# Optimization experiments

Measured on AMD Instinct MI355X. Metric: run time of the kernel, lower is better.

The kernel has to match this reference:

```python
import jax, jax.numpy as jnp
import numpy as np

BATCH, N_NODES = 256, 128
NF = MF = 128
EF = AEF = 5


def setup_inputs() -> dict:
    key = jax.random.key(0)
    k = jax.random.split(key, 6)
    afm = jax.random.normal(k[0], (BATCH, N_NODES, NF), dtype=jnp.float32)
    bfm = jax.random.randint(k[1], (BATCH, N_NODES, N_NODES), 0, EF + 1, dtype=jnp.int32)
    a_bfm = jax.random.randint(k[2], (BATCH, N_NODES), 0, AEF + 1, dtype=jnp.int32)
    adj = jax.random.uniform(k[3], (BATCH, N_NODES, N_NODES), dtype=jnp.float32)
    # xavier_uniform for adj_w (ef, mf, nf): fan_in=nf, fan_out=mf per torch convention on last two dims
    lim_w = float(np.sqrt(6.0 / (MF + NF)))
    adj_w = jax.random.uniform(k[4], (EF, MF, NF), minval=-lim_w, maxval=lim_w, dtype=jnp.float32)
    lim_a = float(np.sqrt(6.0 / (AEF + MF)))
    adj_a = jax.random.uniform(k[5], (AEF, MF), minval=-lim_a, maxval=lim_a, dtype=jnp.float32)
    return {"afm": afm, "bfm": bfm, "a_bfm": a_bfm, "adj": adj, "adj_w": adj_w, "adj_a": adj_a}


def reference(afm, bfm, a_bfm, adj, adj_w, adj_a):
    # afm is accepted by the original forward but never used.
    E = adj_w.shape[0] + 1  # zeros row for "no edge" at index 0
    mf, nf = adj_w.shape[1], adj_w.shape[2]
    W_ext = jnp.concatenate([jnp.zeros((1, mf, nf), adj_w.dtype), adj_w], axis=0)  # (E, mf, nf)
    A_ext = jnp.concatenate([jnp.zeros((1, mf), adj_a.dtype), adj_a], axis=0)      # (E_a, mf)
    att = A_ext[a_bfm]  # (b, n, mf); nf == mf required by original matmul
    # Original: msg[b,i,j,m] = sum_k W_ext[bfm[b,i,j], m, k] * att[b, j, k], then sum over i.
    # Contract first per edge type (small), then count-weight instead of gathering huge tensor.
    contrib = jnp.einsum('emn,bjn->bjem', W_ext, att)                  # (b, n, E, mf)
    cnt = jax.nn.one_hot(bfm, E, dtype=contrib.dtype).sum(axis=1)      # (b, j, E) = #{i : bfm[b,i,j]=e}
    messages = jnp.einsum('bje,bjem->bjm', cnt, contrib)               # (b, n, mf)
    return jnp.matmul(adj, messages)                                   # (b, n, mf)
```

## Files before the change

### kernel.cpp

```cpp
#include <hip/hip_runtime.h>

typedef short s16x8 __attribute__((ext_vector_type(8)));
typedef float f32x4 __attribute__((ext_vector_type(4)));
typedef int i32x4 __attribute__((ext_vector_type(4)));

__device__ __forceinline__ short f2bf(float f) {
  union { float f; unsigned u; } cv;
  cv.f = f;
  unsigned u = cv.u;
  u = (u + 0x7FFFu + ((u >> 16) & 1u)) >> 16;
  return (short)u;
}
__device__ __forceinline__ unsigned pk2(float lo, float hi) {
  union { float f; unsigned u; } a, b;
  a.f = lo;
  b.f = hi;
  return (a.u >> 16) | (b.u & 0xFFFF0000u);
}

__global__ __launch_bounds__(256, 4) void hist_mc_kernel(
    const int* __restrict__ bfm, const float* __restrict__ adj_w,
    const float* __restrict__ adj_a, uint2* __restrict__ cnt_h,
    unsigned short* __restrict__ McT) {
  __shared__ unsigned red[4][32][4][2];
  __shared__ float As[5][128];
  const int t = threadIdx.x;

  if (blockIdx.x < 20) {
    const int bi = blockIdx.x;
    const int e = bi >> 2, mg = bi & 3;
    for (int idx = t; idx < 640; idx += 256) As[idx >> 7][idx & 127] = adj_a[idx];
    __syncthreads();
    const int m = mg * 32 + (t >> 3), ns = t & 7;
    const float* W = adj_w + (size_t)e * 16384 + (size_t)m * 128 + ns * 16;
    float acc[5] = {0.f, 0.f, 0.f, 0.f, 0.f};
#pragma unroll
    for (int it = 0; it < 4; ++it) {
      const float4 wv = *(const float4*)(W + it * 4);
      const float wa[4] = {wv.x, wv.y, wv.z, wv.w};
#pragma unroll
      for (int q = 0; q < 4; ++q) {
        const int n = ns * 16 + it * 4 + q;
#pragma unroll
        for (int a = 0; a < 5; ++a) acc[a] = fmaf(wa[q], As[a][n], acc[a]);
      }
    }
#pragma unroll
    for (int d = 1; d < 8; d <<= 1)
#pragma unroll
      for (int a = 0; a < 5; ++a) acc[a] += __shfl_xor(acc[a], d);
    if (ns == 0) {
#pragma unroll
      for (int a = 0; a < 5; ++a)
        McT[m * 40 + e * 5 + a] = (unsigned short)f2bf(acc[a]);
      if (e == 0)
#pragma unroll
        for (int r = 25; r < 40; ++r) McT[m * 40 + r] = 0;
    }
    return;
  }

  const int idx2 = blockIdx.x - 20;
  const int b = idx2 >> 1, hh = idx2 & 1;
  const int w = t >> 6, l = t & 63;
  const i32x4* bp = (const i32x4*)bfm + (size_t)b * 4096 + hh * 2048;
  unsigned pA[4] = {0, 0, 0, 0}, pB[4] = {0, 0, 0, 0};
#pragma unroll
  for (int it = 0; it < 8; ++it) {
    const i32x4 v = __builtin_nontemporal_load(&bp[it * 256 + t]);
#pragma unroll
    for (int jj = 0; jj < 4; ++jj) {
      const int vj = v[jj];
      pA[jj] += (unsigned)(vj == 1) + ((unsigned)(vj == 2) << 8) +
                ((unsigned)(vj == 3) << 16) + ((unsigned)(vj == 4) << 24);
      pB[jj] += (unsigned)(vj == 5);
    }
  }
#pragma unroll
  for (int jj = 0; jj < 4; ++jj) {
    pA[jj] += (unsigned)__shfl_xor((int)pA[jj], 32);
    pB[jj] += (unsigned)__shfl_xor((int)pB[jj], 32);
  }
  if (l < 32) {
#pragma unroll
    for (int jj = 0; jj < 4; ++jj) {
      red[w][l][jj][0] = pA[jj];
      red[w][l][jj][1] = pB[jj];
    }
  }
  __syncthreads();
  if (t < 128) {
    unsigned A = 0, B = 0;
    const int cc = t >> 2, jj = t & 3;
#pragma unroll
    for (int w2 = 0; w2 < 4; ++w2) {
      A += red[w2][cc][jj][0];
      B += red[w2][cc][jj][1];
    }
    cnt_h[(b * 2 + hh) * 128 + t] = make_uint2(A, B);
  }
}

__global__ __launch_bounds__(256, 2) void skinny_kernel(
    const float* __restrict__ adj, const int* __restrict__ a_bfm,
    const uint2* __restrict__ cnt_h, const unsigned short* __restrict__ McT,
    float* __restrict__ out) {
  __shared__ __align__(16) unsigned short Pt[32 * 128];
  __shared__ __align__(16) unsigned short Mt[128 * 40];
  __shared__ __align__(16) unsigned short Qs[4 * 16 * 40];
  const int bh = blockIdx.x, b = bh >> 1, hh = bh & 1;
  const int t = threadIdx.x, w = t >> 6, l = t & 63, g = l >> 4, c = l & 15;
  const int row0 = hh * 64 + w * 16;

  uint2 h0 = make_uint2(0u, 0u), h1 = make_uint2(0u, 0u);
  int av = 0;
  if (t < 128) {
    h0 = cnt_h[(b * 2 + 0) * 128 + t];
    h1 = cnt_h[(b * 2 + 1) * 128 + t];
    av = a_bfm[b * 128 + t];
  }
  s16x8 mst0 = *(const s16x8*)&McT[t * 8];
  s16x8 mst1 = *(const s16x8*)&McT[(256 + t) * 8];
  s16x8 mst2 = {0, 0, 0, 0, 0, 0, 0, 0};
  if (t < 128) mst2 = *(const s16x8*)&McT[(512 + t) * 8];
  const float* arow = adj + (size_t)b * 16384 + (size_t)(row0 + c) * 128;
  f32x4 a0[4], a1[4];
#pragma unroll
  for (int kk = 0; kk < 4; ++kk) {
    a0[kk] = __builtin_nontemporal_load(
        (const f32x4*)(arow + kk * 32 + g * 8));
    a1[kk] = __builtin_nontemporal_load(
        (const f32x4*)(arow + kk * 32 + g * 8 + 4));
  }

  ((uint4*)Pt)[t] = make_uint4(0u, 0u, 0u, 0u);
  ((uint4*)Pt)[256 + t] = make_uint4(0u, 0u, 0u, 0u);
  *(s16x8*)&Mt[t * 8] = mst0;
  *(s16x8*)&Mt[(256 + t) * 8] = mst1;
  if (t < 128) *(s16x8*)&Mt[(512 + t) * 8] = mst2;
  asm volatile("s_waitcnt lgkmcnt(0)" ::: "memory");
  __builtin_amdgcn_s_barrier();

  if (t < 128 && av > 0) {
    const unsigned cx = h0.x + h1.x;
    const unsigned cy = h0.y + h1.y;
    const int ai = av - 1;
    const int chunk = t >> 3, off = t & 7;
    const float cf[5] = {(float)(cx & 255u), (float)((cx >> 8) & 255u),
                         (float)((cx >> 16) & 255u), (float)(cx >> 24),
                         (float)(cy & 255u)};
#pragma unroll
    for (int ei = 0; ei < 5; ++ei) {
      const int r = ei * 5 + ai;
      Pt[r * 128 + ((chunk ^ (r & 15)) << 3) + off] =
          (unsigned short)f2bf(cf[ei]);
    }
  }
  asm volatile("s_waitcnt lgkmcnt(0)" ::: "memory");
  __builtin_amdgcn_s_barrier();

  s16x8 bP[4][2];
#pragma unroll
  for (int kk = 0; kk < 4; ++kk)
#pragma unroll
    for (int ct = 0; ct < 2; ++ct) {
      const int r = ct * 16 + c;
      bP[kk][ct] = *(const s16x8*)&Pt[r * 128 + (((kk * 4 + g) ^ (r & 15)) << 3)];
    }
  s16x8 apk[4];
#pragma unroll
  for (int kk = 0; kk < 4; ++kk) {
    unsigned* pu = (unsigned*)&apk[kk];
    pu[0] = pk2(a0[kk][0], a0[kk][1]);
    pu[1] = pk2(a0[kk][2], a0[kk][3]);
    pu[2] = pk2(a1[kk][0], a1[kk][1]);
    pu[3] = pk2(a1[kk][2], a1[kk][3]);
  }
  f32x4 accQ[2] = {{0.f, 0.f, 0.f, 0.f}, {0.f, 0.f, 0.f, 0.f}};
#pragma unroll
  for (int kk = 0; kk < 4; ++kk)
#pragma unroll
    for (int ct = 0; ct < 2; ++ct)
      accQ[ct] = __builtin_amdgcn_mfma_f32_16x16x32_bf16(apk[kk], bP[kk][ct],
                                                         accQ[ct], 0, 0, 0);

  unsigned short* qsw = &Qs[w * 16 * 40];
#pragma unroll
  for (int ct = 0; ct < 2; ++ct)
#pragma unroll
    for (int q = 0; q < 4; ++q)
      qsw[(g * 4 + q) * 40 + ct * 16 + c] = (unsigned short)f2bf(accQ[ct][q]);
  const s16x8 aQ = *(const s16x8*)&qsw[c * 40 + g * 8];

  float* ob = out + (size_t)b * 16384 + (size_t)row0 * 128;
#pragma unroll
  for (int mt = 0; mt < 8; ++mt) {
    const s16x8 bM = *(const s16x8*)&Mt[(mt * 16 + c) * 40 + g * 8];
    f32x4 acc2 = {0.f, 0.f, 0.f, 0.f};
    acc2 = __builtin_amdgcn_mfma_f32_16x16x32_bf16(aQ, bM, acc2, 0, 0, 0);
#pragma unroll
    for (int q = 0; q < 4; ++q)
      __builtin_nontemporal_store(acc2[q],
                                  &ob[(g * 4 + q) * 128 + mt * 16 + c]);
  }
}

extern "C" void kernel_launch(void* const* d_in, const int* in_sizes, int n_in,
                              void* d_out, int out_size, void* d_ws,
                              size_t ws_size, hipStream_t stream) {
  const int* bfm = (const int*)d_in[1];
  const int* a_bfm = (const int*)d_in[2];
  const float* adj = (const float*)d_in[3];
  const float* adj_w = (const float*)d_in[4];
  const float* adj_a = (const float*)d_in[5];
  float* out = (float*)d_out;

  unsigned short* McT = (unsigned short*)d_ws;
  uint2* cnt_h = (uint2*)((char*)d_ws + 16384);

  hist_mc_kernel<<<dim3(532), dim3(256), 0, stream>>>(bfm, adj_w, adj_a,
                                                      cnt_h, McT);
  skinny_kernel<<<dim3(512), dim3(256), 0, stream>>>(adj, a_bfm, cnt_h, McT,
                                                     out);
}
```

Before: 16.86 us.

## Spread adj_w·adj_a precompute across all histogram blocks instead of dedicated blocks

The 20 dedicated blocks that computed the per-edge-type weight/attention products are removed. Each of the 640 (m,e) dot products is now handled by one wave in waves 0-1 of the 512 histogram blocks, using a 64-lane shuffle reduction. The bfm loads are also issued up front into registers so they overlap with this extra work. This evens out the tail of the first kernel and cuts the grid to 512 blocks, at the cost of more registers and more shuffle work per block.

```diff
diff --git a/kernel.cpp b/kernel.cpp
--- a/kernel.cpp
+++ b/kernel.cpp
@@ -23,54 +23,61 @@
     const float* __restrict__ adj_a, uint2* __restrict__ cnt_h,
     unsigned short* __restrict__ McT) {
   __shared__ unsigned red[4][32][4][2];
-  __shared__ float As[5][128];
   const int t = threadIdx.x;
-
-  if (blockIdx.x < 20) {
-    const int bi = blockIdx.x;
-    const int e = bi >> 2, mg = bi & 3;
-    for (int idx = t; idx < 640; idx += 256) As[idx >> 7][idx & 127] = adj_a[idx];
-    __syncthreads();
-    const int m = mg * 32 + (t >> 3), ns = t & 7;
-    const float* W = adj_w + (size_t)e * 16384 + (size_t)m * 128 + ns * 16;
-    float acc[5] = {0.f, 0.f, 0.f, 0.f, 0.f};
-#pragma unroll
-    for (int it = 0; it < 4; ++it) {
-      const float4 wv = *(const float4*)(W + it * 4);
-      const float wa[4] = {wv.x, wv.y, wv.z, wv.w};
-#pragma unroll
-      for (int q = 0; q < 4; ++q) {
-        const int n = ns * 16 + it * 4 + q;
-#pragma unroll
-        for (int a = 0; a < 5; ++a) acc[a] = fmaf(wa[q], As[a][n], acc[a]);
-      }
-    }
-#pragma unroll
-    for (int d = 1; d < 8; d <<= 1)
+  const int bid = blockIdx.x;
+  const int b = bid >> 1, hh = bid & 1;
+  const int w = t >> 6, l = t & 63;
+
+  int p = -1;
+  float2 wv = make_float2(0.f, 0.f);
+  float2 av2[5];
+#pragma unroll
+  for (int a = 0; a < 5; ++a) av2[a] = make_float2(0.f, 0.f);
+  if (w < 2) {
+    const int pc = bid + (w << 9);
+    if (pc < 640) {
+      p = pc;
+      const int e = pc % 5, m = pc / 5;
+      wv = *(const float2*)(adj_w + (size_t)e * 16384 + (size_t)m * 128 + l * 2);
+#pragma unroll
+      for (int a = 0; a < 5; ++a)
+        av2[a] = *(const float2*)(adj_a + a * 128 + l * 2);
+    }
+  }
+
+  const i32x4* bp = (const i32x4*)bfm + (size_t)b * 4096 + hh * 2048;
+  i32x4 bv[8];
+#pragma unroll
+  for (int it = 0; it < 8; ++it)
+    bv[it] = __builtin_nontemporal_load(&bp[it * 256 + t]);
+
+  if (p >= 0) {
+    float acc[5];
+#pragma unroll
+    for (int a = 0; a < 5; ++a) acc[a] = wv.x * av2[a].x + wv.y * av2[a].y;
+#pragma unroll
+    for (int d = 1; d < 64; d <<= 1)
 #pragma unroll
       for (int a = 0; a < 5; ++a) acc[a] += __shfl_xor(acc[a], d);
-    if (ns == 0) {
+    if (l == 0) {
+      const int e = p % 5, m = p / 5;
 #pragma unroll
       for (int a = 0; a < 5; ++a)
         McT[m * 40 + e * 5 + a] = (unsigned short)f2bf(acc[a]);
-      if (e == 0)
-#pragma unroll
-        for (int r = 25; r < 40; ++r) McT[m * 40 + r] = 0;
-    }
-    return;
-  }
-
-  const int idx2 = blockIdx.x - 20;
-  const int b = idx2 >> 1, hh = idx2 & 1;
-  const int w = t >> 6, l = t & 63;
-  const i32x4* bp = (const i32x4*)bfm + (size_t)b * 4096 + hh * 2048;
+    }
+  }
+  if (bid == 511 && t >= 128) {
+    const int m = t - 128;
+#pragma unroll
+    for (int r = 25; r < 40; ++r) McT[m * 40 + r] = 0;
+  }
+
   unsigned pA[4] = {0, 0, 0, 0}, pB[4] = {0, 0, 0, 0};
 #pragma unroll
   for (int it = 0; it < 8; ++it) {
-    const i32x4 v = __builtin_nontemporal_load(&bp[it * 256 + t]);
 #pragma unroll
     for (int jj = 0; jj < 4; ++jj) {
-      const int vj = v[jj];
+      const int vj = bv[it][jj];
       pA[jj] += (unsigned)(vj == 1) + ((unsigned)(vj == 2) << 8) +
                 ((unsigned)(vj == 3) << 16) + ((unsigned)(vj == 4) << 24);
       pB[jj] += (unsigned)(vj == 5);
@@ -127,10 +134,9 @@
   f32x4 a0[4], a1[4];
 #pragma unroll
   for (int kk = 0; kk < 4; ++kk) {
-    a0[kk] = __builtin_nontemporal_load(
-        (const f32x4*)(arow + kk * 32 + g * 8));
-    a1[kk] = __builtin_nontemporal_load(
-        (const f32x4*)(arow + kk * 32 + g * 8 + 4));
+    a0[kk] = __builtin_nontemporal_load((const f32x4*)(arow + kk * 32 + g * 8));
+    a1[kk] =
+        __builtin_nontemporal_load((const f32x4*)(arow + kk * 32 + g * 8 + 4));
   }
 
   ((uint4*)Pt)[t] = make_uint4(0u, 0u, 0u, 0u);
@@ -218,7 +224,7 @@
   unsigned short* McT = (unsigned short*)d_ws;
   uint2* cnt_h = (uint2*)((char*)d_ws + 16384);
 
-  hist_mc_kernel<<<dim3(532), dim3(256), 0, stream>>>(bfm, adj_w, adj_a,
+  hist_mc_kernel<<<dim3(512), dim3(256), 0, stream>>>(bfm, adj_w, adj_a,
                                                       cnt_h, McT);
   skinny_kernel<<<dim3(512), dim3(256), 0, stream>>>(adj, a_bfm, cnt_h, McT,
                                                      out);
```

New measurement: 16.82 us. About the same (-0.2%).
